# Kernel optimization log

Hardware: AMD Instinct MI355X
Metric: run time of the kernel (lower is better)

The kernel has to match this reference:

```python
import jax, jax.numpy as jnp
import numpy as np

B, C, N, L = 8, 128, 65536, 64  # batch, channels, points, instance labels
D_VAR, D_DIST = 0.5, 1.5
P_VAR, P_DIST, P_REG = 1.0, 1.0, 0.001


def setup_inputs() -> dict:
    key = jax.random.key(0)
    k1, k2 = jax.random.split(key)
    prediction = jax.random.normal(k1, (B, C, N), dtype=jnp.float32)
    label = jax.random.randint(k2, (B, N), 0, L)  # with N=65536 every label in [0,L) appears w.h.p.
    return {"prediction": prediction, "label": label}


def _discriminative_loss(prediction, label):
    # one-hot segment membership  [B, N, L]
    onehot = (label[:, :, None] == jnp.arange(L)).astype(prediction.dtype)
    counts = onehot.sum(1)                                   # [B, L]
    # per-instance embedding means (torch: mean over points per unique label)
    centers = jnp.einsum('bcn,bnl->blc', prediction, onehot) / counts[..., None]  # [B, L, C]

    # --- l_reg: torch center is [K, C, 1]; norm over dim=0 (labels) -> [C], sum / K ---
    l_reg = (jnp.linalg.norm(centers, axis=1).sum(-1) / L).sum()

    # --- var loss (faithful to original: center = mean over CHANNEL dim of each point) ---
    chan_mean = prediction.mean(axis=1, keepdims=True)       # [B, 1, N]
    pnorm = jnp.linalg.norm(prediction - chan_mean, axis=1)  # [B, N]
    v = jax.nn.relu(pnorm - D_VAR) ** 2                      # [B, N]
    per_label = jnp.einsum('bn,bnl->bl', v, onehot) / counts # [B, L]
    var = (per_label.sum(-1) / L).sum()

    # --- dist loss (faithful: square_distance_single gets [K, C], so it computes
    #     pairwise squared distances between the C channel-columns over labels -> [C, C]) ---
    sqn = jnp.sum(centers ** 2, axis=1)                      # [B, C]
    gram = jnp.einsum('blc,bld->bcd', centers, centers)      # [B, C, C]
    sqd = jax.nn.relu(sqn[:, :, None] + sqn[:, None, :] - 2.0 * gram)
    dist = jnp.where(sqd > 0, jnp.sqrt(jnp.where(sqd > 0, sqd, 1.0)), 0.0)  # safe-grad sqrt
    hinge = jax.nn.relu(2.0 * D_DIST - dist) ** 2            # [B, C, C]
    denom = 2.0 * L * (L - 1.0 + 1e-16)
    dist_loss = (hinge.sum((-1, -2)) / denom).sum()

    return P_VAR * var + P_DIST * dist_loss + P_REG * l_reg


def reference(prediction, label):
    return _discriminative_loss(prediction, label)
```

## Files before the change

kernel.cpp:

```cpp
#include <hip/hip_runtime.h>
#include <math.h>

#define BB 8
#define CC 128
#define NN 65536
#define LL 64
#define CHK 128

typedef __attribute__((ext_vector_type(16))) float f32x16;
typedef __attribute__((ext_vector_type(8)))  short s16x8;

union V16 { int4 i; uint4 u; s16x8 s; };

__device__ __forceinline__ unsigned bf16rne(float f) {
    unsigned u = __builtin_bit_cast(unsigned, f);
    return (u + 0x7fffu + ((u >> 16) & 1u)) >> 16;
}
__device__ __forceinline__ unsigned packbf(float lo, float hi) {
    return bf16rne(lo) | (bf16rne(hi) << 16);
}
__device__ __forceinline__ unsigned oh2(int a, int b, int t) {
    return (a == t ? 0x3F80u : 0u) | (b == t ? 0x3F800000u : 0u);
}

__global__ __launch_bounds__(256, 3)
void k1_mfma(const float* __restrict__ pred, const int* __restrict__ label,
             float* __restrict__ gpart, float* __restrict__ gcp, float* __restrict__ gvp,
             int blk_per_b, int nchk)
{
    __shared__ __align__(16) unsigned pred_lds[CC * 64];
    __shared__ __align__(16) int lab_s[2048];
    __shared__ __align__(16) float4 pr[256];
    __shared__ float vacc[LL];
    __shared__ unsigned cnt[LL];

    const int tid  = threadIdx.x;
    const int wv   = tid >> 6;
    const int lane = tid & 63;

    const int b   = blockIdx.x / blk_per_b;
    const int blk = blockIdx.x % blk_per_b;
    const int pts = nchk * CHK;
    const int n0b = blk * pts;

    const float* __restrict__ predb = pred + (size_t)b * CC * NN;
    const int*   __restrict__ labb  = label + (size_t)b * NN + n0b;

    if (tid < LL) { vacc[tid] = 0.f; cnt[tid] = 0u; }
    for (int i = tid; i < (pts >> 2); i += 256)
        *(int4*)&lab_s[4*i] = *(const int4*)(labb + 4*i);
    __syncthreads();

    for (int i = tid; i < pts; i += 256) atomicAdd(&cnt[lab_s[i]], 1u);

    f32x16 acc0, acc1;
    #pragma unroll
    for (int i = 0; i < 16; ++i) { acc0[i] = 0.f; acc1[i] = 0.f; }

    const int src_c = tid & 127;
    const int src_h = tid >> 7;
    const int t0lab = lane & 31;
    const int khalf = lane >> 5;
    const int arow  = (wv << 5) + (lane & 31);

    for (int ch = 0; ch < nchk; ++ch) {
        const int n0 = n0b + ch * CHK;

        const float* gp = predb + (size_t)src_c * NN + n0 + src_h * 64;
        float4 r[16];
        #pragma unroll
        for (int j = 0; j < 16; ++j) r[j] = *(const float4*)(gp + 4*j);
        #pragma unroll
        for (int i = 0; i < 8; ++i) {
            uint4 w;
            w.x = packbf(r[2*i].x,   r[2*i].y);
            w.y = packbf(r[2*i].z,   r[2*i].w);
            w.z = packbf(r[2*i+1].x, r[2*i+1].y);
            w.w = packbf(r[2*i+1].z, r[2*i+1].w);
            const int q  = 8*src_h + i;
            const int qs = q ^ (src_c & 15);
            *(uint4*)&pred_lds[src_c*64 + qs*4] = w;
        }
        __syncthreads();

        #pragma unroll
        for (int ks = 0; ks < 8; ++ks) {
            const int k0 = ks * 16;
            const int q  = (k0 >> 3) + khalf;
            const int qs = q ^ (arow & 15);
            V16 a; a.i = *(const int4*)&pred_lds[arow*64 + qs*4];
            const int lbase = ch*CHK + k0 + (khalf << 3);
            const int4 la = *(const int4*)&lab_s[lbase];
            const int4 lb = *(const int4*)&lab_s[lbase + 4];
            V16 b0, b1;
            b0.u = make_uint4(oh2(la.x,la.y,t0lab), oh2(la.z,la.w,t0lab),
                              oh2(lb.x,lb.y,t0lab), oh2(lb.z,lb.w,t0lab));
            const int t1lab = t0lab + 32;
            b1.u = make_uint4(oh2(la.x,la.y,t1lab), oh2(la.z,la.w,t1lab),
                              oh2(lb.x,lb.y,t1lab), oh2(lb.z,lb.w,t1lab));
            acc0 = __builtin_amdgcn_mfma_f32_32x32x16_bf16(a.s, b0.s, acc0, 0, 0, 0);
            acc1 = __builtin_amdgcn_mfma_f32_32x32x16_bf16(a.s, b1.s, acc1, 0, 0, 0);
        }

        {
            const int p2 = tid & 63;
            float s1a=0.f, s2a=0.f, s1b=0.f, s2b=0.f;
            #pragma unroll
            for (int i2 = 0; i2 < 32; ++i2) {
                const int c  = (wv << 5) + i2;
                const int qs = (p2 >> 2) ^ (c & 15);
                const unsigned u = pred_lds[c*64 + qs*4 + (p2 & 3)];
                const float fa = __builtin_bit_cast(float, u << 16);
                const float fb = __builtin_bit_cast(float, u & 0xffff0000u);
                s1a += fa; s2a = fmaf(fa, fa, s2a);
                s1b += fb; s2b = fmaf(fb, fb, s2b);
            }
            pr[(p2 << 2) | wv] = make_float4(s1a, s2a, s1b, s2b);
        }
        __syncthreads();

        if (tid < 64) {
            const float4 t0 = pr[4*tid], t1 = pr[4*tid+1], t2 = pr[4*tid+2], t3 = pr[4*tid+3];
            const float s1 = t0.x+t1.x+t2.x+t3.x, s2 = t0.y+t1.y+t2.y+t3.y;
            const float u1 = t0.z+t1.z+t2.z+t3.z, u2 = t0.w+t1.w+t2.w+t3.w;
            float sqa = s2 - s1*s1*(1.0f/CC); sqa = sqa > 0.f ? sqa : 0.f;
            float sqb = u2 - u1*u1*(1.0f/CC); sqb = sqb > 0.f ? sqb : 0.f;
            const float da = sqrtf(sqa) - 0.5f, db = sqrtf(sqb) - 0.5f;
            const float va = da > 0.f ? da*da : 0.f, vb = db > 0.f ? db*db : 0.f;
            unsafeAtomicAdd(&vacc[lab_s[ch*CHK + 2*tid]], va);
            unsafeAtomicAdd(&vacc[lab_s[ch*CHK + 2*tid + 1]], vb);
        }
    }
    __syncthreads();

    float* __restrict__ gp0 = gpart + (size_t)blockIdx.x * 8192 + wv*2048 + lane*4;
    #pragma unroll
    for (int j = 0; j < 4; ++j)
        *(float4*)(gp0 + j*256) = make_float4(acc0[4*j], acc0[4*j+1], acc0[4*j+2], acc0[4*j+3]);
    #pragma unroll
    for (int j = 0; j < 4; ++j)
        *(float4*)(gp0 + (j+4)*256) = make_float4(acc1[4*j], acc1[4*j+1], acc1[4*j+2], acc1[4*j+3]);

    if (tid < LL) {
        gcp[blockIdx.x*64 + tid] = (float)cnt[tid];
        gvp[blockIdx.x*64 + tid] = vacc[tid];
    }
}

__global__ __launch_bounds__(256)
void k1b_reduce(const float* __restrict__ gpart, const float* __restrict__ gcp,
                const float* __restrict__ gvp, float* __restrict__ gsum,
                float* __restrict__ gcnt, float* __restrict__ gv, int blk_per_b)
{
    const int kb = blockIdx.x, tid = threadIdx.x;
    if (kb < 256) {
        const int b = kb >> 5, wvj = kb & 31, wv = wvj >> 3, jj = wvj & 7;
        const float* p = gpart + (size_t)b * blk_per_b * 8192 + wv*2048 + jj*256 + tid;
        float s = 0.f;
        for (int k = 0; k < blk_per_b; ++k) s += p[(size_t)k * 8192];
        const int lane = tid >> 2, q = tid & 3;
        const int l   = (lane & 31) + ((jj >> 2) << 5);
        const int r2  = (jj & 3)*4 + q;
        const int chn = (wv << 5) + (r2 & 3) + ((r2 >> 2) << 3) + ((lane >> 5) << 2);
        gsum[b*8192 + l*128 + chn] = s;
    } else {
        const int idx = (kb - 256)*256 + tid;
        const int which = idx >> 9;
        const int o = idx & 511;
        const int b = o >> 6, l = o & 63;
        const float* p = (which ? gvp : gcp) + (size_t)b * blk_per_b * 64 + l;
        float s = 0.f;
        for (int k = 0; k < blk_per_b; ++k) s += p[k*64];
        if (which) gv[o] = s; else gcnt[o] = s;
    }
}

#define CEN_STRIDE 132

__global__ __launch_bounds__(256)
void k2_finalize(const float* __restrict__ gsum, const float* __restrict__ gcnt,
                 const float* __restrict__ gv, float* __restrict__ out)
{
    __shared__ float cen[LL * CEN_STRIDE];
    __shared__ float invc[LL];
    __shared__ float red[256];

    const int tid   = threadIdx.x;
    const int b     = blockIdx.x >> 3;
    const int strip = blockIdx.x & 7;

    if (tid < LL) invc[tid] = 1.0f / gcnt[b * LL + tid];
    __syncthreads();

    const float* __restrict__ gs = gsum + (size_t)b * LL * CC;
    for (int i = tid; i < LL * CC; i += 256) {
        const int l = i >> 7, c = i & 127;
        cen[l * CEN_STRIDE + c] = gs[i] * invc[l];
    }
    __syncthreads();

    const int c  = strip * 16 + (tid >> 4);
    const int d0 = (tid & 15) * 8;

    float areg[LL];
    #pragma unroll
    for (int l = 0; l < LL; ++l) areg[l] = cen[l * CEN_STRIDE + c];

    float sqd[8] = {0.f, 0.f, 0.f, 0.f, 0.f, 0.f, 0.f, 0.f};
    #pragma unroll
    for (int l = 0; l < LL; ++l) {
        const float4 b0 = *(const float4*)&cen[l * CEN_STRIDE + d0];
        const float4 b1 = *(const float4*)&cen[l * CEN_STRIDE + d0 + 4];
        const float a = areg[l];
        float t;
        t = a - b0.x; sqd[0] += t * t;
        t = a - b0.y; sqd[1] += t * t;
        t = a - b0.z; sqd[2] += t * t;
        t = a - b0.w; sqd[3] += t * t;
        t = a - b1.x; sqd[4] += t * t;
        t = a - b1.y; sqd[5] += t * t;
        t = a - b1.z; sqd[6] += t * t;
        t = a - b1.w; sqd[7] += t * t;
    }

    float hsum = 0.f;
    #pragma unroll
    for (int j = 0; j < 8; ++j) {
        const float dist = sqd[j] > 0.f ? sqrtf(sqd[j]) : 0.f;
        float h = 3.0f - dist;
        h = h > 0.f ? h : 0.f;
        hsum += h * h;
    }
    float my = hsum * (1.0f / 8064.0f);

    if (strip == 0) {
        if (tid < CC) {
            float s = 0.f;
            #pragma unroll
            for (int l = 0; l < LL; ++l) {
                const float v = cen[l * CEN_STRIDE + tid];
                s += v * v;
            }
            my += 0.001f * sqrtf(s) * (1.0f / LL);
        }
        if (tid < LL) {
            my += gv[b * LL + tid] * invc[tid] * (1.0f / LL);
        }
    }

    red[tid] = my;
    __syncthreads();
    for (int s = 128; s > 0; s >>= 1) {
        if (tid < s) red[tid] += red[tid + s];
        __syncthreads();
    }
    if (tid == 0) unsafeAtomicAdd(out, red[0]);
}

extern "C" void kernel_launch(void* const* d_in, const int* in_sizes, int n_in,
                              void* d_out, int out_size, void* d_ws, size_t ws_size,
                              hipStream_t stream) {
    (void)in_sizes; (void)n_in; (void)out_size;
    const float* pred  = (const float*)d_in[0];
    const int*   label = (const int*)d_in[1];
    float* out = (float*)d_out;

    const size_t need64 = ((size_t)512*8192 + (size_t)512*128 + 65536 + 1024) * sizeof(float);
    const int blk_per_b = (ws_size >= need64) ? 64 : 32;
    const int nchk      = (NN / CHK) / blk_per_b;
    const int nblk      = BB * blk_per_b;

    float* gpart = (float*)d_ws;
    float* gcp   = gpart + (size_t)nblk * 8192;
    float* gvp   = gcp + (size_t)nblk * 64;
    float* gsum  = gvp + (size_t)nblk * 64;
    float* gcnt  = gsum + BB * LL * CC;
    float* gv    = gcnt + BB * LL;

    hipMemsetAsync(d_out, 0, sizeof(float), stream);

    k1_mfma<<<nblk, 256, 0, stream>>>(pred, label, gpart, gcp, gvp, blk_per_b, nchk);
    k1b_reduce<<<260, 256, 0, stream>>>(gpart, gcp, gvp, gsum, gcnt, gv, blk_per_b);
    k2_finalize<<<BB * 8, 256, 0, stream>>>(gsum, gcnt, gv, out);
}
```

Measured before the change: 419.5 us.

## Prefetch next prediction chunk into registers and lighten block barriers

Software-pipelines the main MFMA kernel: the global loads for the next chunk of predictions are issued into registers before the current chunk is written to LDS and consumed, so global latency overlaps the compute. __syncthreads is replaced by an explicit lgkmcnt wait plus s_barrier, which leaves outstanding global loads in flight across the barrier. Label staging is also loaded directly into registers, and the per-point partial-sum buffer becomes struct-of-arrays. Occupancy is lowered from 3 to 2 blocks per CU to fit the extra registers, and the output memset is folded into the reduce kernel to save a launch.

```diff
diff --git a/kernel.cpp b/kernel.cpp
--- a/kernel.cpp
+++ b/kernel.cpp
@@ -23,14 +23,20 @@
     return (a == t ? 0x3F80u : 0u) | (b == t ? 0x3F800000u : 0u);
 }
 
-__global__ __launch_bounds__(256, 3)
+#define BAR_LGKM() do { \
+    asm volatile("s_waitcnt lgkmcnt(0)" ::: "memory"); \
+    __builtin_amdgcn_s_barrier(); \
+    asm volatile("" ::: "memory"); \
+} while (0)
+
+__global__ __launch_bounds__(256, 2)
 void k1_mfma(const float* __restrict__ pred, const int* __restrict__ label,
              float* __restrict__ gpart, float* __restrict__ gcp, float* __restrict__ gvp,
              int blk_per_b, int nchk)
 {
     __shared__ __align__(16) unsigned pred_lds[CC * 64];
     __shared__ __align__(16) int lab_s[2048];
-    __shared__ __align__(16) float4 pr[256];
+    __shared__ float prS[4][256];
     __shared__ float vacc[LL];
     __shared__ unsigned cnt[LL];
 
@@ -46,50 +52,64 @@
     const float* __restrict__ predb = pred + (size_t)b * CC * NN;
     const int*   __restrict__ labb  = label + (size_t)b * NN + n0b;
 
-    if (tid < LL) { vacc[tid] = 0.f; cnt[tid] = 0u; }
-    for (int i = tid; i < (pts >> 2); i += 256)
-        *(int4*)&lab_s[4*i] = *(const int4*)(labb + 4*i);
-    __syncthreads();
-
-    for (int i = tid; i < pts; i += 256) atomicAdd(&cnt[lab_s[i]], 1u);
-
-    f32x16 acc0, acc1;
-    #pragma unroll
-    for (int i = 0; i < 16; ++i) { acc0[i] = 0.f; acc1[i] = 0.f; }
-
     const int src_c = tid & 127;
     const int src_h = tid >> 7;
+    const float* __restrict__ gpbase = predb + (size_t)src_c * NN + n0b + src_h * 64;
+
+    const int4* __restrict__ labv = (const int4*)labb;
+    int4 lv0 = labv[tid];
+    int4 lv1 = make_int4(0, 0, 0, 0);
+    const bool two = (pts > 1024);
+    if (two) lv1 = labv[tid + 256];
+
+    float4 r[16];
+    #pragma unroll
+    for (int j = 0; j < 16; ++j) r[j] = *(const float4*)(gpbase + 4 * j);
+
+    if (tid < LL) { vacc[tid] = 0.f; cnt[tid] = 0u; }
+    *(int4*)&lab_s[4 * tid] = lv0;
+    if (two) *(int4*)&lab_s[4 * (tid + 256)] = lv1;
+    BAR_LGKM();
+
+    for (int i = tid; i < pts; i += 256) atomicAdd(&cnt[lab_s[i]], 1u);
+
+    f32x16 acc0, acc1;
+    #pragma unroll
+    for (int i = 0; i < 16; ++i) { acc0[i] = 0.f; acc1[i] = 0.f; }
+
     const int t0lab = lane & 31;
     const int khalf = lane >> 5;
     const int arow  = (wv << 5) + (lane & 31);
 
     for (int ch = 0; ch < nchk; ++ch) {
-        const int n0 = n0b + ch * CHK;
-
-        const float* gp = predb + (size_t)src_c * NN + n0 + src_h * 64;
-        float4 r[16];
-        #pragma unroll
-        for (int j = 0; j < 16; ++j) r[j] = *(const float4*)(gp + 4*j);
+        uint4 w[8];
         #pragma unroll
         for (int i = 0; i < 8; ++i) {
-            uint4 w;
-            w.x = packbf(r[2*i].x,   r[2*i].y);
-            w.y = packbf(r[2*i].z,   r[2*i].w);
-            w.z = packbf(r[2*i+1].x, r[2*i+1].y);
-            w.w = packbf(r[2*i+1].z, r[2*i+1].w);
-            const int q  = 8*src_h + i;
+            w[i].x = packbf(r[2*i].x,   r[2*i].y);
+            w[i].y = packbf(r[2*i].z,   r[2*i].w);
+            w[i].z = packbf(r[2*i+1].x, r[2*i+1].y);
+            w[i].w = packbf(r[2*i+1].z, r[2*i+1].w);
+        }
+        if (ch + 1 < nchk) {
+            const float* gp = gpbase + (ch + 1) * CHK;
+            #pragma unroll
+            for (int j = 0; j < 16; ++j) r[j] = *(const float4*)(gp + 4 * j);
+        }
+        #pragma unroll
+        for (int i = 0; i < 8; ++i) {
+            const int q  = 8 * src_h + i;
             const int qs = q ^ (src_c & 15);
-            *(uint4*)&pred_lds[src_c*64 + qs*4] = w;
-        }
-        __syncthreads();
+            *(uint4*)&pred_lds[src_c * 64 + qs * 4] = w[i];
+        }
+        BAR_LGKM();
 
         #pragma unroll
         for (int ks = 0; ks < 8; ++ks) {
             const int k0 = ks * 16;
             const int q  = (k0 >> 3) + khalf;
             const int qs = q ^ (arow & 15);
-            V16 a; a.i = *(const int4*)&pred_lds[arow*64 + qs*4];
-            const int lbase = ch*CHK + k0 + (khalf << 3);
+            V16 a; a.i = *(const int4*)&pred_lds[arow * 64 + qs * 4];
+            const int lbase = ch * CHK + k0 + (khalf << 3);
             const int4 la = *(const int4*)&lab_s[lbase];
             const int4 lb = *(const int4*)&lab_s[lbase + 4];
             V16 b0, b1;
@@ -115,14 +135,17 @@
                 s1a += fa; s2a = fmaf(fa, fa, s2a);
                 s1b += fb; s2b = fmaf(fb, fb, s2b);
             }
-            pr[(p2 << 2) | wv] = make_float4(s1a, s2a, s1b, s2b);
-        }
-        __syncthreads();
+            const int idx = (wv << 6) | p2;
+            prS[0][idx] = s1a; prS[1][idx] = s2a;
+            prS[2][idx] = s1b; prS[3][idx] = s2b;
+        }
+        BAR_LGKM();
 
         if (tid < 64) {
-            const float4 t0 = pr[4*tid], t1 = pr[4*tid+1], t2 = pr[4*tid+2], t3 = pr[4*tid+3];
-            const float s1 = t0.x+t1.x+t2.x+t3.x, s2 = t0.y+t1.y+t2.y+t3.y;
-            const float u1 = t0.z+t1.z+t2.z+t3.z, u2 = t0.w+t1.w+t2.w+t3.w;
+            const float s1 = prS[0][tid] + prS[0][tid+64] + prS[0][tid+128] + prS[0][tid+192];
+            const float s2 = prS[1][tid] + prS[1][tid+64] + prS[1][tid+128] + prS[1][tid+192];
+            const float u1 = prS[2][tid] + prS[2][tid+64] + prS[2][tid+128] + prS[2][tid+192];
+            const float u2 = prS[3][tid] + prS[3][tid+64] + prS[3][tid+128] + prS[3][tid+192];
             float sqa = s2 - s1*s1*(1.0f/CC); sqa = sqa > 0.f ? sqa : 0.f;
             float sqb = u2 - u1*u1*(1.0f/CC); sqb = sqb > 0.f ? sqb : 0.f;
             const float da = sqrtf(sqa) - 0.5f, db = sqrtf(sqb) - 0.5f;
@@ -150,9 +173,11 @@
 __global__ __launch_bounds__(256)
 void k1b_reduce(const float* __restrict__ gpart, const float* __restrict__ gcp,
                 const float* __restrict__ gvp, float* __restrict__ gsum,
-                float* __restrict__ gcnt, float* __restrict__ gv, int blk_per_b)
+                float* __restrict__ gcnt, float* __restrict__ gv,
+                float* __restrict__ out, int blk_per_b)
 {
     const int kb = blockIdx.x, tid = threadIdx.x;
+    if (kb == 0 && tid == 0) *out = 0.f;
     if (kb < 256) {
         const int b = kb >> 5, wvj = kb & 31, wv = wvj >> 3, jj = wvj & 7;
         const float* p = gpart + (size_t)b * blk_per_b * 8192 + wv*2048 + jj*256 + tid;
@@ -277,9 +302,7 @@
     float* gcnt  = gsum + BB * LL * CC;
     float* gv    = gcnt + BB * LL;
 
-    hipMemsetAsync(d_out, 0, sizeof(float), stream);
-
     k1_mfma<<<nblk, 256, 0, stream>>>(pred, label, gpart, gcp, gvp, blk_per_b, nchk);
-    k1b_reduce<<<260, 256, 0, stream>>>(gpart, gcp, gvp, gsum, gcnt, gv, blk_per_b);
+    k1b_reduce<<<260, 256, 0, stream>>>(gpart, gcp, gvp, gsum, gcnt, gv, out, blk_per_b);
     k2_finalize<<<BB * 8, 256, 0, stream>>>(gsum, gcnt, gv, out);
 }
```

Result: no change. 421.7 us (+0.5%).
